# Optimization experiments

Measured on AMD Instinct MI355X. Metric: run time of the kernel, lower is better.

Reference implementation:

```python
import jax, jax.numpy as jnp
import numpy as np

B, S, D, Q, U = 32, 8192, 256, 256, 128


def setup_inputs() -> dict:
    key = jax.random.key(0)
    k1, k2, k3, k4, k5 = jax.random.split(key, 5)
    query = jax.random.normal(k1, (B, Q), dtype=jnp.float32)
    values = jax.random.normal(k2, (B, S, D), dtype=jnp.float32)
    # Dense kernels (Keras stores as [in, out]); scale ~ Glorot-ish
    W1 = jax.random.normal(k3, (D, U), dtype=jnp.float32) * 0.05
    W2 = jax.random.normal(k4, (Q, U), dtype=jnp.float32) * 0.05
    V = jax.random.normal(k5, (U, 1), dtype=jnp.float32) * 0.05
    return {"query": query, "values": values, "W1": W1, "W2": W2, "V": V}


def reference(query, values, W1, W2, V):
    # score = V^T tanh(W1*values + W2*query)  -> (B, S, 1)
    proj_v = jnp.einsum('bsd,du->bsu', values, W1)          # (B,S,U)
    proj_q = jnp.einsum('bq,qu->bu', query, W2)[:, None, :]  # (B,1,U)
    score = jnp.einsum('bsu,uo->bso', jnp.tanh(proj_v + proj_q), V)  # (B,S,1)
    attention_weights = jax.nn.softmax(score, axis=1)        # softmax over seq_len
    # dropout is identity at inference (training=False)
    context = jnp.sum(attention_weights * values, axis=1)    # (B,D)
    return context, attention_weights
```

## Files before the change

### kernel.cpp

```cpp
#include <hip/hip_runtime.h>
#include <stdint.h>

#define B_ 32
#define S_ 8192
#define D_ 256
#define Q_ 256
#define U_ 128
#define NCHUNK 64

typedef float floatx4 __attribute__((ext_vector_type(4)));
typedef float f32x4 __attribute__((ext_vector_type(4)));
typedef __bf16 bf16x8 __attribute__((ext_vector_type(8)));
typedef unsigned short ushortx4 __attribute__((ext_vector_type(4)));
typedef unsigned short ushortx8 __attribute__((ext_vector_type(8)));

static __device__ __forceinline__ unsigned short f2bf(float f) {
    unsigned int x = __builtin_bit_cast(unsigned int, f);
    x += 0x7FFFu + ((x >> 16) & 1u);
    return (unsigned short)(x >> 16);
}

static __device__ __forceinline__ float bf2f(unsigned short u) {
    unsigned int x = ((unsigned int)u) << 16;
    return __builtin_bit_cast(float, x);
}

static __device__ __forceinline__ float fast_tanh(float x) {
    x = fminf(15.f, fmaxf(-15.f, x));
    float e = __expf(2.f * x);
    return __fdividef(e - 1.f, e + 1.f);
}

__global__ __launch_bounds__(128) void prep_kernel(
        const float* __restrict__ query, const float* __restrict__ W1,
        const float* __restrict__ W2, float* __restrict__ pq,
        unsigned short* __restrict__ w1t) {
    int b = blockIdx.x;
    int t = threadIdx.x;
    __shared__ float qrow[Q_];
    qrow[t] = query[b * Q_ + t];
    qrow[t + 128] = query[b * Q_ + 128 + t];
    __syncthreads();
    float acc = 0.f;
#pragma unroll 8
    for (int q = 0; q < Q_; ++q) acc = fmaf(qrow[q], W2[q * U_ + t], acc);
    pq[b * U_ + t] = acc;
    int base = (b * 128 + t) * 8;
#pragma unroll
    for (int j = 0; j < 8; ++j) {
        int e = base + j;
        int n = e >> 8, k = e & 255;
        w1t[e] = f2bf(W1[k * U_ + n]);
    }
}

__global__ __launch_bounds__(256, 2) void fused_kernel(
        const float* __restrict__ values, const unsigned short* __restrict__ w1t,
        const float* __restrict__ pq, const float* __restrict__ V,
        float* __restrict__ scores, float* __restrict__ mbuf,
        float* __restrict__ lbuf, float* __restrict__ cpart) {
    __shared__ __align__(16) char smem[81920];
    unsigned short* As = (unsigned short*)smem;
    unsigned short* Bs = (unsigned short*)(smem + 65536);
    float* part = (float*)(smem + 65536);
    float* sarr = part + 256;
    float* parr = sarr + 128;
    float* redm = parr + 128;
    floatx4* cbuf = (floatx4*)(smem + 65536 + 4096);

    int b = blockIdx.y;
    int cid = blockIdx.x;
    int s0 = cid * 128;
    int tid = threadIdx.x;
    int lane = tid & 63;
    int wave = tid >> 6;
    int wr = wave >> 1, wc = wave & 1;
    int cc = lane & 15, qg = lane >> 4;
    int cc7 = cc & 7;

    const float* vb = values + ((size_t)b * S_ + s0) * D_;

    f32x4 acc[4][4];
#pragma unroll
    for (int mt = 0; mt < 4; ++mt)
#pragma unroll
        for (int nt = 0; nt < 4; ++nt) acc[mt][nt] = (f32x4){0.f, 0.f, 0.f, 0.f};

#pragma unroll
    for (int i = 0; i < 32; ++i) {
        int fidx = tid + i * 256;
        int row = fidx >> 6, fc = fidx & 63;
        floatx4 v = *reinterpret_cast<const floatx4*>(vb + (size_t)row * D_ + fc * 4);
        ushortx4 u;
        u[0] = f2bf(v[0]); u[1] = f2bf(v[1]); u[2] = f2bf(v[2]); u[3] = f2bf(v[3]);
        int addr = row * 256 + (((fc >> 1) ^ (row & 7)) << 3) + (fc & 1) * 4;
        *reinterpret_cast<ushortx4*>(&As[addr]) = u;
    }
#pragma unroll
    for (int i = 0; i < 4; ++i) {
        int cidx = tid + i * 256;
        int n = cidx >> 3, kc = cidx & 7;
        ushortx8 w = *reinterpret_cast<const ushortx8*>(&w1t[n * 256 + kc * 8]);
        *reinterpret_cast<ushortx8*>(&Bs[n * 64 + ((kc ^ (n & 7)) << 3)]) = w;
    }
    __syncthreads();

    for (int kt = 0; kt < 4; ++kt) {
#pragma unroll
        for (int ks = 0; ks < 2; ++ks) {
            int ksg = kt * 2 + ks;
            bf16x8 af[4], bfr[4];
#pragma unroll
            for (int mt = 0; mt < 4; ++mt) {
                int r = wr * 64 + mt * 16 + cc;
                af[mt] = *reinterpret_cast<const bf16x8*>(
                    &As[r * 256 + (((ksg * 4 + qg) ^ cc7) << 3)]);
            }
#pragma unroll
            for (int nt = 0; nt < 4; ++nt) {
                int n = wc * 64 + nt * 16 + cc;
                bfr[nt] = *reinterpret_cast<const bf16x8*>(
                    &Bs[n * 64 + (((ks * 4 + qg) ^ cc7) << 3)]);
            }
#pragma unroll
            for (int mt = 0; mt < 4; ++mt)
#pragma unroll
                for (int nt = 0; nt < 4; ++nt)
                    acc[mt][nt] = __builtin_amdgcn_mfma_f32_16x16x32_bf16(
                        af[mt], bfr[nt], acc[mt][nt], 0, 0, 0);
        }
        __syncthreads();
        if (kt < 3) {
            int kt1 = kt + 1;
#pragma unroll
            for (int i = 0; i < 4; ++i) {
                int cidx = tid + i * 256;
                int n = cidx >> 3, kc = cidx & 7;
                ushortx8 w = *reinterpret_cast<const ushortx8*>(
                    &w1t[n * 256 + kt1 * 64 + kc * 8]);
                *reinterpret_cast<ushortx8*>(&Bs[n * 64 + ((kc ^ (n & 7)) << 3)]) = w;
            }
            __syncthreads();
        }
    }

    float Vu[4], pqu[4];
#pragma unroll
    for (int nt = 0; nt < 4; ++nt) {
        int u = wc * 64 + nt * 16 + cc;
        Vu[nt] = V[u];
        pqu[nt] = pq[b * U_ + u];
    }
#pragma unroll
    for (int mt = 0; mt < 4; ++mt) {
#pragma unroll
        for (int r = 0; r < 4; ++r) {
            float s = 0.f;
#pragma unroll
            for (int nt = 0; nt < 4; ++nt)
                s += Vu[nt] * fast_tanh(acc[mt][nt][r] + pqu[nt]);
            s += __shfl_xor(s, 1);
            s += __shfl_xor(s, 2);
            s += __shfl_xor(s, 4);
            s += __shfl_xor(s, 8);
            if (cc == 0) part[wc * 128 + wr * 64 + mt * 16 + qg * 4 + r] = s;
        }
    }
    __syncthreads();
    if (tid < 128) {
        float sc = part[tid] + part[128 + tid];
        scores[(size_t)b * S_ + s0 + tid] = sc;
        sarr[tid] = sc;
    }
    __syncthreads();
    if (tid < 64) {
        float m = fmaxf(sarr[tid], sarr[tid + 64]);
#pragma unroll
        for (int off = 32; off >= 1; off >>= 1) m = fmaxf(m, __shfl_xor(m, off));
        if (tid == 0) redm[0] = m;
    }
    __syncthreads();
    float M = redm[0];
    if (tid < 128) parr[tid] = __expf(sarr[tid] - M);
    __syncthreads();
    if (tid < 64) {
        float l = parr[tid] + parr[tid + 64];
#pragma unroll
        for (int off = 32; off >= 1; off >>= 1) l += __shfl_xor(l, off);
        if (tid == 0) { mbuf[b * NCHUNK + cid] = M; lbuf[b * NCHUNK + cid] = l; }
    }
    __syncthreads();

    int g = tid & 63, sub = tid >> 6;
    floatx4 acc4 = {0.f, 0.f, 0.f, 0.f};
#pragma unroll 4
    for (int i = 0; i < 32; ++i) {
        int r = i * 4 + sub;
        float w = parr[r];
        int addr = r * 256 + (((g >> 1) ^ (r & 7)) << 3) + (g & 1) * 4;
        ushortx4 u = *reinterpret_cast<const ushortx4*>(&As[addr]);
        acc4[0] = fmaf(bf2f(u[0]), w, acc4[0]);
        acc4[1] = fmaf(bf2f(u[1]), w, acc4[1]);
        acc4[2] = fmaf(bf2f(u[2]), w, acc4[2]);
        acc4[3] = fmaf(bf2f(u[3]), w, acc4[3]);
    }
    cbuf[tid] = acc4;
    __syncthreads();
    if (tid < 64) {
        floatx4 r4 = cbuf[tid] + cbuf[tid + 64] + cbuf[tid + 128] + cbuf[tid + 192];
        *reinterpret_cast<floatx4*>(cpart + ((size_t)b * NCHUNK + cid) * D_ + g * 4) = r4;
    }
}

__global__ __launch_bounds__(256) void finalize_kernel(
        const float* __restrict__ scores, const float* __restrict__ mbuf,
        const float* __restrict__ lbuf, const float* __restrict__ cpart,
        float* __restrict__ out) {
    int b = blockIdx.x;
    int part_id = blockIdx.y;
    int tid = threadIdx.x;
    __shared__ float MZ[2];
    __shared__ float alpha[NCHUNK];
    if (tid < 64) {
        float m = mbuf[b * NCHUNK + tid];
        float l = lbuf[b * NCHUNK + tid];
        float M = m;
#pragma unroll
        for (int off = 32; off >= 1; off >>= 1) M = fmaxf(M, __shfl_xor(M, off));
        float z = l * __expf(m - M);
#pragma unroll
        for (int off = 32; off >= 1; off >>= 1) z += __shfl_xor(z, off);
        if (tid == 0) { MZ[0] = M; MZ[1] = z; }
    }
    __syncthreads();
    float M = MZ[0];
    float invZ = 1.f / MZ[1];

    if (part_id < 8) {
        size_t off = (size_t)b * S_ + part_id * 1024;
        floatx4 v = *reinterpret_cast<const floatx4*>(scores + off + tid * 4);
        floatx4 w;
#pragma unroll
        for (int j = 0; j < 4; ++j) w[j] = __expf(v[j] - M) * invZ;
        *reinterpret_cast<floatx4*>(out + B_ * D_ + off + tid * 4) = w;
    } else {
        if (tid < 64) alpha[tid] = __expf(mbuf[b * NCHUNK + tid] - M) * invZ;
        __syncthreads();
        float acc = 0.f;
#pragma unroll 8
        for (int c = 0; c < NCHUNK; ++c)
            acc = fmaf(alpha[c], cpart[((size_t)b * NCHUNK + c) * D_ + tid], acc);
        out[b * D_ + tid] = acc;
    }
}

extern "C" void kernel_launch(void* const* d_in, const int* in_sizes, int n_in,
                              void* d_out, int out_size, void* d_ws, size_t ws_size,
                              hipStream_t stream) {
    const float* query  = (const float*)d_in[0];
    const float* values = (const float*)d_in[1];
    const float* W1     = (const float*)d_in[2];
    const float* W2     = (const float*)d_in[3];
    const float* V      = (const float*)d_in[4];
    float* out = (float*)d_out;

    char* ws = (char*)d_ws;
    unsigned short* w1t = (unsigned short*)ws;               ws += 65536;
    float* pq     = (float*)ws;                              ws += 16384;
    float* scores = (float*)ws;                              ws += B_ * S_ * 4;
    float* mbuf   = (float*)ws;                              ws += B_ * NCHUNK * 4;
    float* lbuf   = (float*)ws;                              ws += B_ * NCHUNK * 4;
    float* cpart  = (float*)ws;

    prep_kernel<<<dim3(32), dim3(128), 0, stream>>>(query, W1, W2, pq, w1t);
    fused_kernel<<<dim3(NCHUNK, B_), dim3(256), 0, stream>>>(values, w1t, pq, V,
                                                             scores, mbuf, lbuf, cpart);
    finalize_kernel<<<dim3(B_, 9), dim3(256), 0, stream>>>(scores, mbuf, lbuf, cpart, out);
}
```

Baseline: 417.3 us.

## Halve chunk size, raise occupancy, and register-prefetch K tiles of values and W1

Each block now handles 64 sequence rows instead of 128, so there are twice as many chunks and shared memory drops to 48KB, allowing 3 blocks per CU. Values and W1 tiles are loaded per K-slice into registers one stage ahead and written to LDS after each compute step, which overlaps global loads with MFMA work instead of staging the whole tile up front. W1 is stored pre-tiled per K-slice, and the finalize kernel reduces across 128 chunk partials with a two-wave max/sum. The cost is more partial results to combine and more register pressure from the prefetch buffers.

New measurement: 391.3 us. -6.2%, faster.

```diff
diff --git a/kernel.cpp b/kernel.cpp
--- a/kernel.cpp
+++ b/kernel.cpp
@@ -6,7 +6,7 @@
 #define D_ 256
 #define Q_ 256
 #define U_ 128
-#define NCHUNK 64
+#define NCHUNK 128
 
 typedef float floatx4 __attribute__((ext_vector_type(4)));
 typedef float f32x4 __attribute__((ext_vector_type(4)));
@@ -50,27 +50,27 @@
     for (int j = 0; j < 8; ++j) {
         int e = base + j;
         int n = e >> 8, k = e & 255;
-        w1t[e] = f2bf(W1[k * U_ + n]);
-    }
-}
-
-__global__ __launch_bounds__(256, 2) void fused_kernel(
+        w1t[(k >> 6) * 8192 + n * 64 + (k & 63)] = f2bf(W1[k * U_ + n]);
+    }
+}
+
+__global__ __launch_bounds__(256, 3) void fused_kernel(
         const float* __restrict__ values, const unsigned short* __restrict__ w1t,
         const float* __restrict__ pq, const float* __restrict__ V,
         float* __restrict__ scores, float* __restrict__ mbuf,
         float* __restrict__ lbuf, float* __restrict__ cpart) {
-    __shared__ __align__(16) char smem[81920];
+    __shared__ __align__(16) char smem[49152];
     unsigned short* As = (unsigned short*)smem;
-    unsigned short* Bs = (unsigned short*)(smem + 65536);
-    float* part = (float*)(smem + 65536);
-    float* sarr = part + 256;
-    float* parr = sarr + 128;
-    float* redm = parr + 128;
-    floatx4* cbuf = (floatx4*)(smem + 65536 + 4096);
+    unsigned short* Bs = (unsigned short*)(smem + 32768);
+    float* part = (float*)(smem + 32768);
+    float* sarr = part + 128;
+    float* parr = sarr + 64;
+    float* redm = parr + 64;
+    floatx4* cbuf = (floatx4*)(smem + 32768 + 4096);
 
     int b = blockIdx.y;
     int cid = blockIdx.x;
-    int s0 = cid * 128;
+    int s0 = cid * 64;
     int tid = threadIdx.x;
     int lane = tid & 63;
     int wave = tid >> 6;
@@ -80,39 +80,63 @@
 
     const float* vb = values + ((size_t)b * S_ + s0) * D_;
 
-    f32x4 acc[4][4];
-#pragma unroll
-    for (int mt = 0; mt < 4; ++mt)
+    f32x4 acc[2][4];
+#pragma unroll
+    for (int mt = 0; mt < 2; ++mt)
 #pragma unroll
         for (int nt = 0; nt < 4; ++nt) acc[mt][nt] = (f32x4){0.f, 0.f, 0.f, 0.f};
 
-#pragma unroll
-    for (int i = 0; i < 32; ++i) {
-        int fidx = tid + i * 256;
-        int row = fidx >> 6, fc = fidx & 63;
-        floatx4 v = *reinterpret_cast<const floatx4*>(vb + (size_t)row * D_ + fc * 4);
-        ushortx4 u;
-        u[0] = f2bf(v[0]); u[1] = f2bf(v[1]); u[2] = f2bf(v[2]); u[3] = f2bf(v[3]);
-        int addr = row * 256 + (((fc >> 1) ^ (row & 7)) << 3) + (fc & 1) * 4;
-        *reinterpret_cast<ushortx4*>(&As[addr]) = u;
-    }
-#pragma unroll
-    for (int i = 0; i < 4; ++i) {
-        int cidx = tid + i * 256;
-        int n = cidx >> 3, kc = cidx & 7;
-        ushortx8 w = *reinterpret_cast<const ushortx8*>(&w1t[n * 256 + kc * 8]);
-        *reinterpret_cast<ushortx8*>(&Bs[n * 64 + ((kc ^ (n & 7)) << 3)]) = w;
-    }
-    __syncthreads();
-
+    floatx4 areg[4];
+    ushortx8 breg[4];
+    int arow = tid >> 4, afc = tid & 15;
+    int bn = tid >> 3, bkc = tid & 7;
+
+    auto load_a = [&](int kt) {
+#pragma unroll
+        for (int i = 0; i < 4; ++i) {
+            int row = arow + i * 16;
+            areg[i] = *reinterpret_cast<const floatx4*>(vb + (size_t)row * D_ + kt * 64 + afc * 4);
+        }
+    };
+    auto load_b = [&](int kt) {
+#pragma unroll
+        for (int i = 0; i < 4; ++i) {
+            int cidx = tid + i * 256;
+            breg[i] = *reinterpret_cast<const ushortx8*>(&w1t[kt * 8192 + cidx * 8]);
+        }
+    };
+    auto write_ab = [&](int kt) {
+#pragma unroll
+        for (int i = 0; i < 4; ++i) {
+            int row = arow + i * 16;
+            ushortx4 u;
+            u[0] = f2bf(areg[i][0]); u[1] = f2bf(areg[i][1]);
+            u[2] = f2bf(areg[i][2]); u[3] = f2bf(areg[i][3]);
+            int chunk16 = kt * 8 + (afc >> 1);
+            int addr = row * 256 + ((chunk16 ^ (row & 7)) << 3) + (afc & 1) * 4;
+            *reinterpret_cast<ushortx4*>(&As[addr]) = u;
+        }
+#pragma unroll
+        for (int i = 0; i < 4; ++i) {
+            int n = bn + i * 32;
+            *reinterpret_cast<ushortx8*>(&Bs[n * 64 + ((bkc ^ (n & 7)) << 3)]) = breg[i];
+        }
+    };
+
+    load_a(0); load_b(0);
+    write_ab(0);
+    load_a(1); load_b(1);
+    __syncthreads();
+
+#pragma unroll
     for (int kt = 0; kt < 4; ++kt) {
 #pragma unroll
         for (int ks = 0; ks < 2; ++ks) {
             int ksg = kt * 2 + ks;
-            bf16x8 af[4], bfr[4];
-#pragma unroll
-            for (int mt = 0; mt < 4; ++mt) {
-                int r = wr * 64 + mt * 16 + cc;
+            bf16x8 af[2], bfr[4];
+#pragma unroll
+            for (int mt = 0; mt < 2; ++mt) {
+                int r = wr * 32 + mt * 16 + cc;
                 af[mt] = *reinterpret_cast<const bf16x8*>(
                     &As[r * 256 + (((ksg * 4 + qg) ^ cc7) << 3)]);
             }
@@ -123,7 +147,7 @@
                     &Bs[n * 64 + (((ks * 4 + qg) ^ cc7) << 3)]);
             }
 #pragma unroll
-            for (int mt = 0; mt < 4; ++mt)
+            for (int mt = 0; mt < 2; ++mt)
 #pragma unroll
                 for (int nt = 0; nt < 4; ++nt)
                     acc[mt][nt] = __builtin_amdgcn_mfma_f32_16x16x32_bf16(
@@ -131,15 +155,8 @@
         }
         __syncthreads();
         if (kt < 3) {
-            int kt1 = kt + 1;
-#pragma unroll
-            for (int i = 0; i < 4; ++i) {
-                int cidx = tid + i * 256;
-                int n = cidx >> 3, kc = cidx & 7;
-                ushortx8 w = *reinterpret_cast<const ushortx8*>(
-                    &w1t[n * 256 + kt1 * 64 + kc * 8]);
-                *reinterpret_cast<ushortx8*>(&Bs[n * 64 + ((kc ^ (n & 7)) << 3)]) = w;
-            }
+            write_ab(kt + 1);
+            if (kt < 2) { load_a(kt + 2); load_b(kt + 2); }
             __syncthreads();
         }
     }
@@ -152,7 +169,7 @@
         pqu[nt] = pq[b * U_ + u];
     }
 #pragma unroll
-    for (int mt = 0; mt < 4; ++mt) {
+    for (int mt = 0; mt < 2; ++mt) {
 #pragma unroll
         for (int r = 0; r < 4; ++r) {
             float s = 0.f;
@@ -163,28 +180,28 @@
             s += __shfl_xor(s, 2);
             s += __shfl_xor(s, 4);
             s += __shfl_xor(s, 8);
-            if (cc == 0) part[wc * 128 + wr * 64 + mt * 16 + qg * 4 + r] = s;
-        }
-    }
-    __syncthreads();
-    if (tid < 128) {
-        float sc = part[tid] + part[128 + tid];
+            if (cc == 0) part[wc * 64 + wr * 32 + mt * 16 + qg * 4 + r] = s;
+        }
+    }
+    __syncthreads();
+    if (tid < 64) {
+        float sc = part[tid] + part[64 + tid];
         scores[(size_t)b * S_ + s0 + tid] = sc;
         sarr[tid] = sc;
     }
     __syncthreads();
     if (tid < 64) {
-        float m = fmaxf(sarr[tid], sarr[tid + 64]);
+        float m = sarr[tid];
 #pragma unroll
         for (int off = 32; off >= 1; off >>= 1) m = fmaxf(m, __shfl_xor(m, off));
         if (tid == 0) redm[0] = m;
     }
     __syncthreads();
     float M = redm[0];
-    if (tid < 128) parr[tid] = __expf(sarr[tid] - M);
-    __syncthreads();
-    if (tid < 64) {
-        float l = parr[tid] + parr[tid + 64];
+    if (tid < 64) parr[tid] = __expf(sarr[tid] - M);
+    __syncthreads();
+    if (tid < 64) {
+        float l = parr[tid];
 #pragma unroll
         for (int off = 32; off >= 1; off >>= 1) l += __shfl_xor(l, off);
         if (tid == 0) { mbuf[b * NCHUNK + cid] = M; lbuf[b * NCHUNK + cid] = l; }
@@ -194,7 +211,7 @@
     int g = tid & 63, sub = tid >> 6;
     floatx4 acc4 = {0.f, 0.f, 0.f, 0.f};
 #pragma unroll 4
-    for (int i = 0; i < 32; ++i) {
+    for (int i = 0; i < 16; ++i) {
         int r = i * 4 + sub;
         float w = parr[r];
         int addr = r * 256 + (((g >> 1) ^ (r & 7)) << 3) + (g & 1) * 4;
@@ -219,22 +236,24 @@
     int b = blockIdx.x;
     int part_id = blockIdx.y;
     int tid = threadIdx.x;
-    __shared__ float MZ[2];
+    __shared__ float wred[4];
     __shared__ float alpha[NCHUNK];
-    if (tid < 64) {
+    if (tid < NCHUNK) {
         float m = mbuf[b * NCHUNK + tid];
-        float l = lbuf[b * NCHUNK + tid];
-        float M = m;
-#pragma unroll
-        for (int off = 32; off >= 1; off >>= 1) M = fmaxf(M, __shfl_xor(M, off));
-        float z = l * __expf(m - M);
+#pragma unroll
+        for (int off = 32; off >= 1; off >>= 1) m = fmaxf(m, __shfl_xor(m, off));
+        if ((tid & 63) == 0) wred[tid >> 6] = m;
+    }
+    __syncthreads();
+    float M = fmaxf(wred[0], wred[1]);
+    if (tid < NCHUNK) {
+        float z = lbuf[b * NCHUNK + tid] * __expf(mbuf[b * NCHUNK + tid] - M);
 #pragma unroll
         for (int off = 32; off >= 1; off >>= 1) z += __shfl_xor(z, off);
-        if (tid == 0) { MZ[0] = M; MZ[1] = z; }
-    }
-    __syncthreads();
-    float M = MZ[0];
-    float invZ = 1.f / MZ[1];
+        if ((tid & 63) == 0) wred[2 + (tid >> 6)] = z;
+    }
+    __syncthreads();
+    float invZ = 1.f / (wred[2] + wred[3]);
 
     if (part_id < 8) {
         size_t off = (size_t)b * S_ + part_id * 1024;
@@ -244,7 +263,7 @@
         for (int j = 0; j < 4; ++j) w[j] = __expf(v[j] - M) * invZ;
         *reinterpret_cast<floatx4*>(out + B_ * D_ + off + tid * 4) = w;
     } else {
-        if (tid < 64) alpha[tid] = __expf(mbuf[b * NCHUNK + tid] - M) * invZ;
+        if (tid < NCHUNK) alpha[tid] = __expf(mbuf[b * NCHUNK + tid] - M) * invZ;
         __syncthreads();
         float acc = 0.f;
 #pragma unroll 8
```
